# Optimization experiments

Hardware: AMD Instinct MI355X
Metric: run time of the kernel (lower is better)

The kernel has to match this reference:

```python
import jax, jax.numpy as jnp
import numpy as np

N_NODES = 100000
N_EDGES = 1600000
IN_DIM = 64
OUT_DIM = 64


def setup_inputs() -> dict:
    key = jax.random.key(0)
    k_x, k_e, k_wm, k_bm, k_wu, k_bu = jax.random.split(key, 6)
    x = jax.random.normal(k_x, (N_NODES, IN_DIM), dtype=jnp.float32)
    edge_index = jax.random.randint(k_e, (2, N_EDGES), 0, N_NODES, dtype=jnp.int64)
    # PyTorch Linear default init: U(-1/sqrt(fan_in), 1/sqrt(fan_in))
    lim_m = 1.0 / np.sqrt(2 * IN_DIM)
    lim_u = 1.0 / np.sqrt(IN_DIM + OUT_DIM)
    W_msg = jax.random.uniform(k_wm, (2 * IN_DIM, OUT_DIM), jnp.float32, -lim_m, lim_m)
    b_msg = jax.random.uniform(k_bm, (OUT_DIM,), jnp.float32, -lim_m, lim_m)
    W_upd = jax.random.uniform(k_wu, (IN_DIM + OUT_DIM, OUT_DIM), jnp.float32, -lim_u, lim_u)
    b_upd = jax.random.uniform(k_bu, (OUT_DIM,), jnp.float32, -lim_u, lim_u)
    return {"x": x, "edge_index": edge_index, "W_msg": W_msg, "b_msg": b_msg,
            "W_upd": W_upd, "b_upd": b_upd}


def reference(x, edge_index, W_msg, b_msg, W_upd, b_upd):
    num_nodes = x.shape[0]
    source, target = edge_index[0], edge_index[1]
    # gather endpoint features and compute messages: [E, 2*in] -> [E, out]
    edge_feats = jnp.concatenate([x[source], x[target]], axis=-1)
    messages = jax.nn.relu(edge_feats @ W_msg + b_msg)
    # mean aggregation onto target nodes
    agg_sum = jax.ops.segment_sum(messages, target, num_segments=num_nodes)
    counts = jax.ops.segment_sum(jnp.ones_like(target, dtype=x.dtype), target,
                                 num_segments=num_nodes)
    aggregated = agg_sum / jnp.clip(counts, 1.0, None)[:, None]
    # update MLP: [N, in+out] -> [N, out]
    updated = jax.nn.relu(jnp.concatenate([x, aggregated], axis=-1) @ W_upd + b_upd)
    return updated
```

## Files before the change

### kernel.cpp

```cpp
#include <hip/hip_runtime.h>
#include <hip/hip_bf16.h>

#define N_NODES 100000
#define N_EDGES 1600000
#define DIM 64
#define NB 196
#define CAP 9216
#define SMASK 0x1FFFFu

typedef __attribute__((ext_vector_type(8))) short bf16x8;
typedef __attribute__((ext_vector_type(4))) float f32x4;
typedef __attribute__((ext_vector_type(2))) float f32x2;

__device__ __forceinline__ unsigned short f2bs(float f) {
    __hip_bfloat16 h = __float2bfloat16(f);
    return *reinterpret_cast<unsigned short*>(&h);
}

__global__ __launch_bounds__(256) void node_transform(
    const float* __restrict__ x, const float* __restrict__ W_msg,
    const float* __restrict__ b_msg,
    unsigned int* __restrict__ Xs8, unsigned int* __restrict__ Xt8,
    int* __restrict__ bcursor)
{
    __shared__ unsigned short WB[8192];
    const int tid = threadIdx.x;
    const int gtid = blockIdx.x * 256 + tid;
    if (gtid < NB) bcursor[gtid] = gtid * CAP;

    for (int i = tid; i < 8192; i += 256) {
        const int j = i & 7, l = (i >> 3) & 63, kk = (i >> 9) & 1, ct = i >> 10;
        const int k = kk * 32 + ((l >> 4) << 3) + j;
        const int c = ct * 16 + (l & 15);
        WB[i] = f2bs(W_msg[(((c >> 6) << 6) + k) * 64 + (c & 63)]);
    }
    __syncthreads();

    const int lane = tid & 63, w = tid >> 6;
    const int r0 = blockIdx.x * 64 + w * 16;
    if (r0 >= N_NODES) return;

    f32x4 acc[8];
    #pragma unroll
    for (int ct = 0; ct < 8; ++ct) acc[ct] = (f32x4){0.f, 0.f, 0.f, 0.f};

    const int r = r0 + (lane & 15);
    #pragma unroll
    for (int kk = 0; kk < 2; ++kk) {
        const int off = kk * 32 + ((lane >> 4) << 3);
        const float4* xp = reinterpret_cast<const float4*>(&x[r * 64 + off]);
        const float4 p0 = xp[0], p1 = xp[1];
        bf16x8 a;
        a[0] = (short)f2bs(p0.x); a[1] = (short)f2bs(p0.y);
        a[2] = (short)f2bs(p0.z); a[3] = (short)f2bs(p0.w);
        a[4] = (short)f2bs(p1.x); a[5] = (short)f2bs(p1.y);
        a[6] = (short)f2bs(p1.z); a[7] = (short)f2bs(p1.w);
        #pragma unroll
        for (int ct = 0; ct < 8; ++ct) {
            const bf16x8 b = *reinterpret_cast<const bf16x8*>(
                &WB[(((ct << 1) | kk) * 64 + lane) << 3]);
            acc[ct] = __builtin_amdgcn_mfma_f32_16x16x32_bf16(a, b, acc[ct], 0, 0, 0);
        }
    }

    const int fr = lane & 15;
    const int rb = r0 + ((lane >> 4) << 2);
    const float bj0 = b_msg[fr],      bj1 = b_msg[16 + fr];
    const float bj2 = b_msg[32 + fr], bj3 = b_msg[48 + fr];
    #pragma unroll
    for (int q = 0; q < 4; ++q) {
        unsigned int xs = 0;
        xs = (unsigned)__builtin_amdgcn_cvt_pk_fp8_f32(acc[0][q], acc[1][q], (int)xs, false);
        xs = (unsigned)__builtin_amdgcn_cvt_pk_fp8_f32(acc[2][q], acc[3][q], (int)xs, true);
        Xs8[(rb + q) * 16 + fr] = xs;
        unsigned int xt = 0;
        xt = (unsigned)__builtin_amdgcn_cvt_pk_fp8_f32(acc[4][q] + bj0, acc[5][q] + bj1, (int)xt, false);
        xt = (unsigned)__builtin_amdgcn_cvt_pk_fp8_f32(acc[6][q] + bj2, acc[7][q] + bj3, (int)xt, true);
        Xt8[(rb + q) * 16 + fr] = xt;
    }
}

__global__ __launch_bounds__(256) void partition(const int* __restrict__ eidx,
                                                 int* __restrict__ bcursor,
                                                 unsigned int* __restrict__ pairs)
{
    __shared__ unsigned int sbuf[4096];
    __shared__ int dbase[4096];
    __shared__ int tcnt[NB], toff[NB], gpos[NB];
    __shared__ int wsum[4];
    const int tid = threadIdx.x, lane = tid & 63, wid = tid >> 6;
    const int base = blockIdx.x * 4096;
    const int tcount = min(4096, N_EDGES - base);
    if (tid < NB) tcnt[tid] = 0;
    __syncthreads();

    unsigned int pk[16]; int bb[16]; int rk[16];
    #pragma unroll
    for (int j = 0; j < 16; ++j) {
        const int idx = base + j * 256 + tid;
        bb[j] = -1;
        if (idx < N_EDGES) {
            const int sv = eidx[idx];
            const int tv = eidx[N_EDGES + idx];
            bb[j] = tv >> 9;
            pk[j] = (unsigned)sv | ((unsigned)(tv & 511) << 17);
            rk[j] = atomicAdd(&tcnt[bb[j]], 1);
        }
    }
    __syncthreads();

    const int v = (tid < NB) ? tcnt[tid] : 0;
    int s = v;
    #pragma unroll
    for (int d = 1; d < 64; d <<= 1) { int u = __shfl_up(s, d); if (lane >= d) s += u; }
    if (lane == 63) wsum[wid] = s;
    __syncthreads();
    if (wid == 0) {
        int ws = (lane < 4) ? wsum[lane] : 0;
        #pragma unroll
        for (int d = 1; d < 4; d <<= 1) { int u = __shfl_up(ws, d); if (lane >= d) ws += u; }
        if (lane < 4) wsum[lane] = ws;
    }
    __syncthreads();
    const int exc = (wid ? wsum[wid - 1] : 0) + s - v;
    if (tid < NB) {
        toff[tid] = exc;
        gpos[tid] = v ? atomicAdd(&bcursor[tid], v) : 0;
    }
    __syncthreads();

    #pragma unroll
    for (int j = 0; j < 16; ++j) {
        if (bb[j] >= 0) {
            const int l = toff[bb[j]] + rk[j];
            sbuf[l]  = pk[j];
            dbase[l] = gpos[bb[j]] + rk[j];
        }
    }
    __syncthreads();
    for (int i = tid; i < tcount; i += 256)
        pairs[dbase[i]] = sbuf[i];
}

__global__ __launch_bounds__(512) void bucket_sort(const int* __restrict__ bcursor,
                                                   const unsigned int* __restrict__ pairs,
                                                   int* __restrict__ csr,
                                                   int* __restrict__ deg,
                                                   int* __restrict__ row)
{
    __shared__ unsigned int ebuf[CAP];
    __shared__ unsigned short rbuf[CAP];
    __shared__ int ncnt[512], noff[512];
    __shared__ int wsum[8];
    const int tid = threadIdx.x, lane = tid & 63, wid = tid >> 6;
    const int b = blockIdx.x;
    const int s0 = b * CAP;
    const int cnt = bcursor[b] - s0;
    ncnt[tid] = 0;
    __syncthreads();

    for (int i = tid; i < cnt; i += 512) {
        const unsigned int p = pairs[s0 + i];
        ebuf[i] = p;
        rbuf[i] = (unsigned short)atomicAdd(&ncnt[p >> 17], 1);
    }
    __syncthreads();

    const int v = ncnt[tid];
    int s = v;
    #pragma unroll
    for (int d = 1; d < 64; d <<= 1) { int u = __shfl_up(s, d); if (lane >= d) s += u; }
    if (lane == 63) wsum[wid] = s;
    __syncthreads();
    if (wid == 0) {
        int ws = (lane < 8) ? wsum[lane] : 0;
        #pragma unroll
        for (int d = 1; d < 8; d <<= 1) { int u = __shfl_up(ws, d); if (lane >= d) ws += u; }
        if (lane < 8) wsum[lane] = ws;
    }
    __syncthreads();
    const int exc = (wid ? wsum[wid - 1] : 0) + s - v;
    noff[tid] = exc;
    const int n = b * 512 + tid;
    if (n < N_NODES) { deg[n] = v; row[n] = s0 + exc; }
    __syncthreads();

    for (int i = tid; i < cnt; i += 512) {
        const unsigned int p = ebuf[i];
        csr[s0 + noff[p >> 17] + (int)rbuf[i]] = (int)(p & SMASK);
    }
}

__device__ __forceinline__ void acc_fp8(unsigned int u,
    float t0, float t1, float t2, float t3,
    float& a0, float& a1, float& a2, float& a3)
{
    const f32x2 lo = __builtin_amdgcn_cvt_pk_f32_fp8(u, false);
    const f32x2 hi = __builtin_amdgcn_cvt_pk_f32_fp8(u, true);
    a0 += fmaxf(lo.x + t0, 0.f);
    a1 += fmaxf(lo.y + t1, 0.f);
    a2 += fmaxf(hi.x + t2, 0.f);
    a3 += fmaxf(hi.y + t3, 0.f);
}

__global__ __launch_bounds__(256) void aggregate(
    const int* __restrict__ row, const int* __restrict__ deg,
    const int* __restrict__ csr,
    const unsigned int* __restrict__ Xs8, const unsigned int* __restrict__ Xt8,
    uint2* __restrict__ aggP)
{
    const int n = blockIdx.x * 4 + (threadIdx.x >> 6);
    const int lane = threadIdx.x & 63;
    if (n >= N_NODES) return;
    const int c = lane & 15, q = lane >> 4;
    const int start = row[n], d = deg[n];
    const unsigned int tp = Xt8[n * 16 + c];
    const f32x2 tlo = __builtin_amdgcn_cvt_pk_f32_fp8(tp, false);
    const f32x2 thi = __builtin_amdgcn_cvt_pk_f32_fp8(tp, true);
    const float t0 = tlo.x, t1 = tlo.y, t2 = thi.x, t3 = thi.y;
    float a0 = 0.f, a1 = 0.f, a2 = 0.f, a3 = 0.f;

    if (d > 0) {
        int i = 0;
        for (; i + 32 <= d; i += 32) {
            int sv[8];
            #pragma unroll
            for (int k = 0; k < 8; ++k) sv[k] = csr[start + i + 4 * k + q];
            unsigned int u[8];
            #pragma unroll
            for (int k = 0; k < 8; ++k) u[k] = Xs8[sv[k] * 16 + c];
            #pragma unroll
            for (int k = 0; k < 8; ++k) acc_fp8(u[k], t0, t1, t2, t3, a0, a1, a2, a3);
        }
        const int rem = d - i;
        if (rem > 0) {
            const int lastIdx = start + d - 1;
            int sv[8]; bool vm[8];
            #pragma unroll
            for (int k = 0; k < 8; ++k) {
                const int e = i + 4 * k + q;
                vm[k] = (e < d);
                sv[k] = csr[vm[k] ? (start + e) : lastIdx];
            }
            unsigned int u[8];
            #pragma unroll
            for (int k = 0; k < 8; ++k) u[k] = Xs8[sv[k] * 16 + c];
            #pragma unroll
            for (int k = 0; k < 8; ++k) {
                const f32x2 lo = __builtin_amdgcn_cvt_pk_f32_fp8(u[k], false);
                const f32x2 hi = __builtin_amdgcn_cvt_pk_f32_fp8(u[k], true);
                if (vm[k]) {
                    a0 += fmaxf(lo.x + t0, 0.f);
                    a1 += fmaxf(lo.y + t1, 0.f);
                    a2 += fmaxf(hi.x + t2, 0.f);
                    a3 += fmaxf(hi.y + t3, 0.f);
                }
            }
        }
    }

    a0 += __shfl_xor(a0, 16); a0 += __shfl_xor(a0, 32);
    a1 += __shfl_xor(a1, 16); a1 += __shfl_xor(a1, 32);
    a2 += __shfl_xor(a2, 16); a2 += __shfl_xor(a2, 32);
    a3 += __shfl_xor(a3, 16); a3 += __shfl_xor(a3, 32);
    if (q == 0) {
        const float inv = (d > 0) ? 1.0f / (float)d : 0.f;
        uint2 v;
        v.x = (unsigned)f2bs(a0 * inv) | ((unsigned)f2bs(a1 * inv) << 16);
        v.y = (unsigned)f2bs(a2 * inv) | ((unsigned)f2bs(a3 * inv) << 16);
        aggP[n * 16 + c] = v;
    }
}

__global__ __launch_bounds__(256) void node_update(
    const float* __restrict__ x, const uint2* __restrict__ aggP,
    const float* __restrict__ W_upd, const float* __restrict__ b_upd,
    float* __restrict__ out)
{
    __shared__ unsigned short WB[8192];
    const int tid = threadIdx.x;
    for (int i = tid; i < 8192; i += 256) {
        const int j = i & 7, l = (i >> 3) & 63, kk = (i >> 9) & 3, ct = i >> 11;
        const int hi = l >> 4;
        int k;
        if (kk < 2) k = kk * 32 + (hi << 3) + j;
        else        k = 64 + ((j & 3) << 4) + ((kk - 2) << 3) + (hi << 1) + (j >> 2);
        const int c = ct * 16 + (l & 15);
        WB[i] = f2bs(W_upd[k * 64 + c]);
    }
    __syncthreads();

    const int lane = tid & 63, w = tid >> 6;
    const int r0 = blockIdx.x * 64 + w * 16;
    if (r0 >= N_NODES) return;

    f32x4 acc[4];
    #pragma unroll
    for (int ct = 0; ct < 4; ++ct) acc[ct] = (f32x4){0.f, 0.f, 0.f, 0.f};

    const int fr = lane & 15, hi = lane >> 4;
    const int r = r0 + fr;
    #pragma unroll
    for (int kk = 0; kk < 4; ++kk) {
        bf16x8 a;
        if (kk < 2) {
            const float4* xp = reinterpret_cast<const float4*>(
                &x[r * 64 + kk * 32 + (hi << 3)]);
            const float4 p0 = xp[0], p1 = xp[1];
            a[0] = (short)f2bs(p0.x); a[1] = (short)f2bs(p0.y);
            a[2] = (short)f2bs(p0.z); a[3] = (short)f2bs(p0.w);
            a[4] = (short)f2bs(p1.x); a[5] = (short)f2bs(p1.y);
            a[6] = (short)f2bs(p1.z); a[7] = (short)f2bs(p1.w);
        } else {
            a = *reinterpret_cast<const bf16x8*>(
                &aggP[r * 16 + ((kk - 2) << 3) + (hi << 1)]);
        }
        #pragma unroll
        for (int ct = 0; ct < 4; ++ct) {
            const bf16x8 b = *reinterpret_cast<const bf16x8*>(
                &WB[(((ct << 2) | kk) * 64 + lane) << 3]);
            acc[ct] = __builtin_amdgcn_mfma_f32_16x16x32_bf16(a, b, acc[ct], 0, 0, 0);
        }
    }

    const int rb = r0 + (hi << 2);
    #pragma unroll
    for (int ct = 0; ct < 4; ++ct) {
        const int cc = ct * 16 + fr;
        const float bj = b_upd[cc];
        #pragma unroll
        for (int qq = 0; qq < 4; ++qq)
            out[(rb + qq) * 64 + cc] = fmaxf(acc[ct][qq] + bj, 0.f);
    }
}

extern "C" void kernel_launch(void* const* d_in, const int* in_sizes, int n_in,
                              void* d_out, int out_size, void* d_ws, size_t ws_size,
                              hipStream_t stream) {
    const float* x     = (const float*)d_in[0];
    const int*   eidx  = (const int*)  d_in[1];
    const float* W_msg = (const float*)d_in[2];
    const float* b_msg = (const float*)d_in[3];
    const float* W_upd = (const float*)d_in[4];
    const float* b_upd = (const float*)d_in[5];
    float* out = (float*)d_out;

    int* deg     = (int*)d_ws;
    int* row     = deg + N_NODES;
    int* bcursor = row + N_NODES;
    unsigned int* pairs = (unsigned int*)(bcursor + 256);
    int* csr     = (int*)(pairs + NB * CAP);
    unsigned int* Xs8 = (unsigned int*)(csr + NB * CAP);
    unsigned int* Xt8 = Xs8 + (size_t)N_NODES * 16;
    uint2* aggP  = (uint2*)(Xt8 + (size_t)N_NODES * 16);

    const int nodeBlocks = (N_NODES + 63) / 64;
    const int partBlocks = (N_EDGES + 4095) / 4096;

    node_transform<<<nodeBlocks, 256, 0, stream>>>(x, W_msg, b_msg, Xs8, Xt8, bcursor);
    partition<<<partBlocks, 256, 0, stream>>>(eidx, bcursor, pairs);
    bucket_sort<<<NB, 512, 0, stream>>>(bcursor, pairs, csr, deg, row);
    aggregate<<<(N_NODES + 3) / 4, 256, 0, stream>>>(row, deg, csr, Xs8, Xt8, aggP);
    node_update<<<nodeBlocks, 256, 0, stream>>>(x, aggP, W_upd, b_upd, out);
}
```

Measured before the change: 119.1 us.

## Fuse node transform with edge partition and store aggregates in fp8

Merges the node transform and edge partition kernels into one launch whose blocks split by index into partition work and transform work. The bucket cursor reset moves to a memset, and cursors now hold relative counts. The aggregated features are stored as fp8 instead of bf16, halving that intermediate's traffic, then widened back to bf16 in the update GEMM. This saves one launch and lets the two independent stages overlap, at the cost of an extra memset and lower precision on the aggregated values.

```diff
diff --git a/kernel.cpp b/kernel.cpp
--- a/kernel.cpp
+++ b/kernel.cpp
@@ -7,6 +7,8 @@
 #define NB 196
 #define CAP 9216
 #define SMASK 0x1FFFFu
+#define PBLOCKS 391
+#define TBLOCKS 1563
 
 typedef __attribute__((ext_vector_type(8))) short bf16x8;
 typedef __attribute__((ext_vector_type(4))) float f32x4;
@@ -17,129 +19,129 @@
     return *reinterpret_cast<unsigned short*>(&h);
 }
 
-__global__ __launch_bounds__(256) void node_transform(
+__global__ __launch_bounds__(256) void transform_partition(
     const float* __restrict__ x, const float* __restrict__ W_msg,
     const float* __restrict__ b_msg,
     unsigned int* __restrict__ Xs8, unsigned int* __restrict__ Xt8,
-    int* __restrict__ bcursor)
-{
-    __shared__ unsigned short WB[8192];
-    const int tid = threadIdx.x;
-    const int gtid = blockIdx.x * 256 + tid;
-    if (gtid < NB) bcursor[gtid] = gtid * CAP;
-
-    for (int i = tid; i < 8192; i += 256) {
-        const int j = i & 7, l = (i >> 3) & 63, kk = (i >> 9) & 1, ct = i >> 10;
-        const int k = kk * 32 + ((l >> 4) << 3) + j;
-        const int c = ct * 16 + (l & 15);
-        WB[i] = f2bs(W_msg[(((c >> 6) << 6) + k) * 64 + (c & 63)]);
-    }
-    __syncthreads();
-
-    const int lane = tid & 63, w = tid >> 6;
-    const int r0 = blockIdx.x * 64 + w * 16;
-    if (r0 >= N_NODES) return;
-
-    f32x4 acc[8];
-    #pragma unroll
-    for (int ct = 0; ct < 8; ++ct) acc[ct] = (f32x4){0.f, 0.f, 0.f, 0.f};
-
-    const int r = r0 + (lane & 15);
-    #pragma unroll
-    for (int kk = 0; kk < 2; ++kk) {
-        const int off = kk * 32 + ((lane >> 4) << 3);
-        const float4* xp = reinterpret_cast<const float4*>(&x[r * 64 + off]);
-        const float4 p0 = xp[0], p1 = xp[1];
-        bf16x8 a;
-        a[0] = (short)f2bs(p0.x); a[1] = (short)f2bs(p0.y);
-        a[2] = (short)f2bs(p0.z); a[3] = (short)f2bs(p0.w);
-        a[4] = (short)f2bs(p1.x); a[5] = (short)f2bs(p1.y);
-        a[6] = (short)f2bs(p1.z); a[7] = (short)f2bs(p1.w);
-        #pragma unroll
-        for (int ct = 0; ct < 8; ++ct) {
-            const bf16x8 b = *reinterpret_cast<const bf16x8*>(
-                &WB[(((ct << 1) | kk) * 64 + lane) << 3]);
-            acc[ct] = __builtin_amdgcn_mfma_f32_16x16x32_bf16(a, b, acc[ct], 0, 0, 0);
-        }
-    }
-
-    const int fr = lane & 15;
-    const int rb = r0 + ((lane >> 4) << 2);
-    const float bj0 = b_msg[fr],      bj1 = b_msg[16 + fr];
-    const float bj2 = b_msg[32 + fr], bj3 = b_msg[48 + fr];
-    #pragma unroll
-    for (int q = 0; q < 4; ++q) {
-        unsigned int xs = 0;
-        xs = (unsigned)__builtin_amdgcn_cvt_pk_fp8_f32(acc[0][q], acc[1][q], (int)xs, false);
-        xs = (unsigned)__builtin_amdgcn_cvt_pk_fp8_f32(acc[2][q], acc[3][q], (int)xs, true);
-        Xs8[(rb + q) * 16 + fr] = xs;
-        unsigned int xt = 0;
-        xt = (unsigned)__builtin_amdgcn_cvt_pk_fp8_f32(acc[4][q] + bj0, acc[5][q] + bj1, (int)xt, false);
-        xt = (unsigned)__builtin_amdgcn_cvt_pk_fp8_f32(acc[6][q] + bj2, acc[7][q] + bj3, (int)xt, true);
-        Xt8[(rb + q) * 16 + fr] = xt;
-    }
-}
-
-__global__ __launch_bounds__(256) void partition(const int* __restrict__ eidx,
-                                                 int* __restrict__ bcursor,
-                                                 unsigned int* __restrict__ pairs)
-{
-    __shared__ unsigned int sbuf[4096];
-    __shared__ int dbase[4096];
-    __shared__ int tcnt[NB], toff[NB], gpos[NB];
-    __shared__ int wsum[4];
+    const int* __restrict__ eidx, int* __restrict__ bcursor,
+    unsigned int* __restrict__ pairs)
+{
+    __shared__ __align__(16) char smem[35200];
     const int tid = threadIdx.x, lane = tid & 63, wid = tid >> 6;
-    const int base = blockIdx.x * 4096;
-    const int tcount = min(4096, N_EDGES - base);
-    if (tid < NB) tcnt[tid] = 0;
-    __syncthreads();
-
-    unsigned int pk[16]; int bb[16]; int rk[16];
-    #pragma unroll
-    for (int j = 0; j < 16; ++j) {
-        const int idx = base + j * 256 + tid;
-        bb[j] = -1;
-        if (idx < N_EDGES) {
-            const int sv = eidx[idx];
-            const int tv = eidx[N_EDGES + idx];
-            bb[j] = tv >> 9;
-            pk[j] = (unsigned)sv | ((unsigned)(tv & 511) << 17);
-            rk[j] = atomicAdd(&tcnt[bb[j]], 1);
-        }
-    }
-    __syncthreads();
-
-    const int v = (tid < NB) ? tcnt[tid] : 0;
-    int s = v;
-    #pragma unroll
-    for (int d = 1; d < 64; d <<= 1) { int u = __shfl_up(s, d); if (lane >= d) s += u; }
-    if (lane == 63) wsum[wid] = s;
-    __syncthreads();
-    if (wid == 0) {
-        int ws = (lane < 4) ? wsum[lane] : 0;
-        #pragma unroll
-        for (int d = 1; d < 4; d <<= 1) { int u = __shfl_up(ws, d); if (lane >= d) ws += u; }
-        if (lane < 4) wsum[lane] = ws;
-    }
-    __syncthreads();
-    const int exc = (wid ? wsum[wid - 1] : 0) + s - v;
-    if (tid < NB) {
-        toff[tid] = exc;
-        gpos[tid] = v ? atomicAdd(&bcursor[tid], v) : 0;
-    }
-    __syncthreads();
-
-    #pragma unroll
-    for (int j = 0; j < 16; ++j) {
-        if (bb[j] >= 0) {
-            const int l = toff[bb[j]] + rk[j];
-            sbuf[l]  = pk[j];
-            dbase[l] = gpos[bb[j]] + rk[j];
-        }
-    }
-    __syncthreads();
-    for (int i = tid; i < tcount; i += 256)
-        pairs[dbase[i]] = sbuf[i];
+
+    if (blockIdx.x >= PBLOCKS) {
+        unsigned short* WB = reinterpret_cast<unsigned short*>(smem);
+        const int tb = blockIdx.x - PBLOCKS;
+
+        for (int i = tid; i < 8192; i += 256) {
+            const int j = i & 7, l = (i >> 3) & 63, kk = (i >> 9) & 1, ct = i >> 10;
+            const int k = kk * 32 + ((l >> 4) << 3) + j;
+            const int c = ct * 16 + (l & 15);
+            WB[i] = f2bs(W_msg[(((c >> 6) << 6) + k) * 64 + (c & 63)]);
+        }
+        __syncthreads();
+
+        const int r0 = tb * 64 + wid * 16;
+        if (r0 >= N_NODES) return;
+
+        f32x4 acc[8];
+        #pragma unroll
+        for (int ct = 0; ct < 8; ++ct) acc[ct] = (f32x4){0.f, 0.f, 0.f, 0.f};
+
+        const int r = r0 + (lane & 15);
+        #pragma unroll
+        for (int kk = 0; kk < 2; ++kk) {
+            const int off = kk * 32 + ((lane >> 4) << 3);
+            const float4* xp = reinterpret_cast<const float4*>(&x[r * 64 + off]);
+            const float4 p0 = xp[0], p1 = xp[1];
+            bf16x8 a;
+            a[0] = (short)f2bs(p0.x); a[1] = (short)f2bs(p0.y);
+            a[2] = (short)f2bs(p0.z); a[3] = (short)f2bs(p0.w);
+            a[4] = (short)f2bs(p1.x); a[5] = (short)f2bs(p1.y);
+            a[6] = (short)f2bs(p1.z); a[7] = (short)f2bs(p1.w);
+            #pragma unroll
+            for (int ct = 0; ct < 8; ++ct) {
+                const bf16x8 b = *reinterpret_cast<const bf16x8*>(
+                    &WB[(((ct << 1) | kk) * 64 + lane) << 3]);
+                acc[ct] = __builtin_amdgcn_mfma_f32_16x16x32_bf16(a, b, acc[ct], 0, 0, 0);
+            }
+        }
+
+        const int fr = lane & 15;
+        const int rb = r0 + ((lane >> 4) << 2);
+        const float bj0 = b_msg[fr],      bj1 = b_msg[16 + fr];
+        const float bj2 = b_msg[32 + fr], bj3 = b_msg[48 + fr];
+        #pragma unroll
+        for (int q = 0; q < 4; ++q) {
+            unsigned int xs = 0;
+            xs = (unsigned)__builtin_amdgcn_cvt_pk_fp8_f32(acc[0][q], acc[1][q], (int)xs, false);
+            xs = (unsigned)__builtin_amdgcn_cvt_pk_fp8_f32(acc[2][q], acc[3][q], (int)xs, true);
+            Xs8[(rb + q) * 16 + fr] = xs;
+            unsigned int xt = 0;
+            xt = (unsigned)__builtin_amdgcn_cvt_pk_fp8_f32(acc[4][q] + bj0, acc[5][q] + bj1, (int)xt, false);
+            xt = (unsigned)__builtin_amdgcn_cvt_pk_fp8_f32(acc[6][q] + bj2, acc[7][q] + bj3, (int)xt, true);
+            Xt8[(rb + q) * 16 + fr] = xt;
+        }
+    } else {
+        unsigned int* sbuf = reinterpret_cast<unsigned int*>(smem);
+        int* dbase = reinterpret_cast<int*>(smem + 16384);
+        int* tcnt  = reinterpret_cast<int*>(smem + 32768);
+        int* toff  = tcnt + NB;
+        int* gpos  = toff + NB;
+        int* wsum  = gpos + NB;
+
+        const int base = blockIdx.x * 4096;
+        const int tcount = min(4096, N_EDGES - base);
+        if (tid < NB) tcnt[tid] = 0;
+        __syncthreads();
+
+        unsigned int pk[16]; int bb[16]; int rk[16];
+        #pragma unroll
+        for (int j = 0; j < 16; ++j) {
+            const int idx = base + j * 256 + tid;
+            bb[j] = -1;
+            if (idx < N_EDGES) {
+                const int sv = eidx[idx];
+                const int tv = eidx[N_EDGES + idx];
+                bb[j] = tv >> 9;
+                pk[j] = (unsigned)sv | ((unsigned)(tv & 511) << 17);
+                rk[j] = atomicAdd(&tcnt[bb[j]], 1);
+            }
+        }
+        __syncthreads();
+
+        const int v = (tid < NB) ? tcnt[tid] : 0;
+        int s = v;
+        #pragma unroll
+        for (int d = 1; d < 64; d <<= 1) { int u = __shfl_up(s, d); if (lane >= d) s += u; }
+        if (lane == 63) wsum[wid] = s;
+        __syncthreads();
+        if (wid == 0) {
+            int ws = (lane < 4) ? wsum[lane] : 0;
+            #pragma unroll
+            for (int d = 1; d < 4; d <<= 1) { int u = __shfl_up(ws, d); if (lane >= d) ws += u; }
+            if (lane < 4) wsum[lane] = ws;
+        }
+        __syncthreads();
+        const int exc = (wid ? wsum[wid - 1] : 0) + s - v;
+        if (tid < NB) {
+            toff[tid] = exc;
+            gpos[tid] = tid * CAP + (v ? atomicAdd(&bcursor[tid], v) : 0);
+        }
+        __syncthreads();
+
+        #pragma unroll
+        for (int j = 0; j < 16; ++j) {
+            if (bb[j] >= 0) {
+                const int l = toff[bb[j]] + rk[j];
+                sbuf[l]  = pk[j];
+                dbase[l] = gpos[bb[j]] + rk[j];
+            }
+        }
+        __syncthreads();
+        for (int i = tid; i < tcount; i += 256)
+            pairs[dbase[i]] = sbuf[i];
+    }
 }
 
 __global__ __launch_bounds__(512) void bucket_sort(const int* __restrict__ bcursor,
@@ -155,7 +157,7 @@
     const int tid = threadIdx.x, lane = tid & 63, wid = tid >> 6;
     const int b = blockIdx.x;
     const int s0 = b * CAP;
-    const int cnt = bcursor[b] - s0;
+    const int cnt = bcursor[b];
     ncnt[tid] = 0;
     __syncthreads();
 
@@ -207,7 +209,7 @@
     const int* __restrict__ row, const int* __restrict__ deg,
     const int* __restrict__ csr,
     const unsigned int* __restrict__ Xs8, const unsigned int* __restrict__ Xt8,
-    uint2* __restrict__ aggP)
+    unsigned int* __restrict__ agg8)
 {
     const int n = blockIdx.x * 4 + (threadIdx.x >> 6);
     const int lane = threadIdx.x & 63;
@@ -265,15 +267,15 @@
     a3 += __shfl_xor(a3, 16); a3 += __shfl_xor(a3, 32);
     if (q == 0) {
         const float inv = (d > 0) ? 1.0f / (float)d : 0.f;
-        uint2 v;
-        v.x = (unsigned)f2bs(a0 * inv) | ((unsigned)f2bs(a1 * inv) << 16);
-        v.y = (unsigned)f2bs(a2 * inv) | ((unsigned)f2bs(a3 * inv) << 16);
-        aggP[n * 16 + c] = v;
+        unsigned int v = 0;
+        v = (unsigned)__builtin_amdgcn_cvt_pk_fp8_f32(a0 * inv, a1 * inv, (int)v, false);
+        v = (unsigned)__builtin_amdgcn_cvt_pk_fp8_f32(a2 * inv, a3 * inv, (int)v, true);
+        agg8[n * 16 + c] = v;
     }
 }
 
 __global__ __launch_bounds__(256) void node_update(
-    const float* __restrict__ x, const uint2* __restrict__ aggP,
+    const float* __restrict__ x, const unsigned int* __restrict__ agg8,
     const float* __restrict__ W_upd, const float* __restrict__ b_upd,
     float* __restrict__ out)
 {
@@ -312,8 +314,17 @@
             a[4] = (short)f2bs(p1.x); a[5] = (short)f2bs(p1.y);
             a[6] = (short)f2bs(p1.z); a[7] = (short)f2bs(p1.w);
         } else {
-            a = *reinterpret_cast<const bf16x8*>(
-                &aggP[r * 16 + ((kk - 2) << 3) + (hi << 1)]);
+            const int off = ((kk - 2) << 3) + (hi << 1);
+            const unsigned int u0 = agg8[r * 16 + off];
+            const unsigned int u1 = agg8[r * 16 + off + 1];
+            const f32x2 l0 = __builtin_amdgcn_cvt_pk_f32_fp8(u0, false);
+            const f32x2 h0 = __builtin_amdgcn_cvt_pk_f32_fp8(u0, true);
+            const f32x2 l1 = __builtin_amdgcn_cvt_pk_f32_fp8(u1, false);
+            const f32x2 h1 = __builtin_amdgcn_cvt_pk_f32_fp8(u1, true);
+            a[0] = (short)f2bs(l0.x); a[1] = (short)f2bs(l0.y);
+            a[2] = (short)f2bs(h0.x); a[3] = (short)f2bs(h0.y);
+            a[4] = (short)f2bs(l1.x); a[5] = (short)f2bs(l1.y);
+            a[6] = (short)f2bs(h1.x); a[7] = (short)f2bs(h1.y);
         }
         #pragma unroll
         for (int ct = 0; ct < 4; ++ct) {
@@ -352,14 +363,12 @@
     int* csr     = (int*)(pairs + NB * CAP);
     unsigned int* Xs8 = (unsigned int*)(csr + NB * CAP);
     unsigned int* Xt8 = Xs8 + (size_t)N_NODES * 16;
-    uint2* aggP  = (uint2*)(Xt8 + (size_t)N_NODES * 16);
-
-    const int nodeBlocks = (N_NODES + 63) / 64;
-    const int partBlocks = (N_EDGES + 4095) / 4096;
-
-    node_transform<<<nodeBlocks, 256, 0, stream>>>(x, W_msg, b_msg, Xs8, Xt8, bcursor);
-    partition<<<partBlocks, 256, 0, stream>>>(eidx, bcursor, pairs);
+    unsigned int* agg8 = Xt8 + (size_t)N_NODES * 16;
+
+    hipMemsetAsync(bcursor, 0, NB * sizeof(int), stream);
+    transform_partition<<<PBLOCKS + TBLOCKS, 256, 0, stream>>>(
+        x, W_msg, b_msg, Xs8, Xt8, eidx, bcursor, pairs);
     bucket_sort<<<NB, 512, 0, stream>>>(bcursor, pairs, csr, deg, row);
-    aggregate<<<(N_NODES + 3) / 4, 256, 0, stream>>>(row, deg, csr, Xs8, Xt8, aggP);
-    node_update<<<nodeBlocks, 256, 0, stream>>>(x, aggP, W_upd, b_upd, out);
-}
+    aggregate<<<(N_NODES + 3) / 4, 256, 0, stream>>>(row, deg, csr, Xs8, Xt8, agg8);
+    node_update<<<(N_NODES + 63) / 64, 256, 0, stream>>>(x, agg8, W_upd, b_upd, out);
+}
```

Result: faster. 110.8 us (-6.9%).
